# Kernel tuning notes

Measured on AMD Instinct MI355X. Metric: run time of the kernel, lower is better.

The kernel has to match this reference:

```python
import jax, jax.numpy as jnp
import numpy as np

B, T, C, H = 4, 2048, 1024, 16
D = C // H  # head_dim = 64


def setup_inputs() -> dict:
    key = jax.random.key(0)
    k1, k2, k3 = jax.random.split(key, 3)
    x = jax.random.normal(k1, (B, T, C), dtype=jnp.float32)
    w_attn = jax.random.normal(k2, (C, 3 * C), dtype=jnp.float32) * (1.0 / np.sqrt(C))
    b_attn = jnp.zeros((3 * C,), dtype=jnp.float32)
    w_proj = jax.random.normal(k3, (C, C), dtype=jnp.float32) * (1.0 / np.sqrt(C))
    b_proj = jnp.zeros((C,), dtype=jnp.float32)
    return {"x": x, "w_attn": w_attn, "b_attn": b_attn, "w_proj": w_proj, "b_proj": b_proj}


def reference(x, w_attn, b_attn, w_proj, b_proj):
    Bx, Tx, Cx = x.shape
    qkv = x @ w_attn + b_attn                      # (B, T, 3C)
    q, k, v = jnp.split(qkv, 3, axis=2)
    # (B, T, C) -> (B, H, T, D)
    q = q.reshape(Bx, Tx, H, D).transpose(0, 2, 1, 3)
    k = k.reshape(Bx, Tx, H, D).transpose(0, 2, 1, 3)
    v = v.reshape(Bx, Tx, H, D).transpose(0, 2, 1, 3)
    scores = jnp.einsum('bhqd,bhkd->bhqk', q, k) / jnp.sqrt(jnp.float32(D))
    causal = jnp.tril(jnp.ones((Tx, Tx), dtype=bool))
    scores = jnp.where(causal[None, None], scores, jnp.float32(-jnp.inf))
    probs = jax.nn.softmax(scores, axis=-1)
    out = jnp.einsum('bhqk,bhkd->bhqd', probs, v)  # (B, H, T, D)
    out = out.transpose(0, 2, 1, 3).reshape(Bx, Tx, Cx)
    return out @ w_proj + b_proj
```

## Files before the change

kernel.cpp:

```cpp
#include <hip/hip_runtime.h>

#define AS1 __attribute__((address_space(1)))
#define AS3 __attribute__((address_space(3)))

using bf16x8  = __attribute__((ext_vector_type(8))) __bf16;
using floatx4 = __attribute__((ext_vector_type(4))) float;

#define SCQ 0.18033688f

__device__ inline ushort f2b(float f) {
    __bf16 h = (__bf16)f;
    return __builtin_bit_cast(ushort, h);
}

__global__ void k_conv(const float* __restrict__ in, ushort* __restrict__ out, int n) {
    int i = (blockIdx.x * 256 + threadIdx.x) * 4;
    if (i < n) {
        float4 v = *(const float4*)(in + i);
        ushort4 o;
        o.x = f2b(v.x); o.y = f2b(v.y); o.z = f2b(v.z); o.w = f2b(v.w);
        *(ushort4*)(out + i) = o;
    }
}

__global__ void k_transpose(const float* __restrict__ in, ushort* __restrict__ out,
                            int R, int Ncol, float scale, int scale_cols) {
    __shared__ float tile[32][33];
    int tx = threadIdx.x & 31, ty = threadIdx.x >> 5;
    int c0 = blockIdx.x * 32, r0 = blockIdx.y * 32;
    for (int i = 0; i < 32; i += 8)
        tile[ty + i][tx] = in[(size_t)(r0 + ty + i) * Ncol + c0 + tx];
    __syncthreads();
    for (int i = 0; i < 32; i += 8) {
        int n = c0 + ty + i;
        float v = tile[tx][ty + i];
        if (n < scale_cols) v *= scale;
        out[(size_t)n * R + r0 + tx] = f2b(v);
    }
}

__global__ __launch_bounds__(256, 2) void k_gemm_bt(
    const ushort* __restrict__ A, const ushort* __restrict__ Bt,
    const float* __restrict__ bias, float* __restrict__ outv,
    int M, int N, int K)
{
    __shared__ __align__(16) ushort As[128 * 32];
    __shared__ __align__(16) ushort Bs[128 * 32];
    int tid = threadIdx.x;
    int m0 = blockIdx.y * 128, n0 = blockIdx.x * 128;
    int lane = tid & 63;
    int wm = (tid >> 7) * 64;
    int wn = ((tid >> 6) & 1) * 64;
    int lr = lane & 15, quad = lane >> 4, lk = quad * 8;

    floatx4 acc[4][4] = {};
    const ushort* ag = A  + (size_t)(m0 + (tid >> 2)) * K + (tid & 3) * 8;
    const ushort* bg = Bt + (size_t)(n0 + (tid >> 2)) * K + (tid & 3) * 8;
    ushort* asd = &As[tid * 8];
    ushort* bsd = &Bs[tid * 8];

    for (int kt = 0; kt < K; kt += 32) {
        __builtin_amdgcn_global_load_lds((const AS1 unsigned int*)(ag + kt),                  (AS3 unsigned int*)(asd),        16, 0, 0);
        __builtin_amdgcn_global_load_lds((const AS1 unsigned int*)(ag + kt + (size_t)64 * K), (AS3 unsigned int*)(asd + 2048), 16, 0, 0);
        __builtin_amdgcn_global_load_lds((const AS1 unsigned int*)(bg + kt),                  (AS3 unsigned int*)(bsd),        16, 0, 0);
        __builtin_amdgcn_global_load_lds((const AS1 unsigned int*)(bg + kt + (size_t)64 * K), (AS3 unsigned int*)(bsd + 2048), 16, 0, 0);
        asm volatile("s_waitcnt vmcnt(0)" ::: "memory");
        __syncthreads();
        bf16x8 af[4], bf[4];
        #pragma unroll
        for (int i = 0; i < 4; ++i) af[i] = *(const bf16x8*)&As[(wm + 16 * i + lr) * 32 + lk];
        #pragma unroll
        for (int j = 0; j < 4; ++j) bf[j] = *(const bf16x8*)&Bs[(wn + 16 * j + lr) * 32 + lk];
        #pragma unroll
        for (int i = 0; i < 4; ++i)
            #pragma unroll
            for (int j = 0; j < 4; ++j)
                acc[i][j] = __builtin_amdgcn_mfma_f32_16x16x32_bf16(af[i], bf[j], acc[i][j], 0, 0, 0);
        __syncthreads();
    }

    #pragma unroll
    for (int j = 0; j < 4; ++j) {
        int col = n0 + wn + 16 * j + lr;
        float bv = bias[col];
        #pragma unroll
        for (int i = 0; i < 4; ++i) {
            int row = m0 + wm + 16 * i + quad * 4;
            #pragma unroll
            for (int r = 0; r < 4; ++r)
                outv[(size_t)(row + r) * N + col] = acc[i][j][r] + bv;
        }
    }
}

__global__ __launch_bounds__(256, 2) void k_gemm_qkv(
    const ushort* __restrict__ A, const ushort* __restrict__ Bt,
    const float* __restrict__ bias, ushort* __restrict__ qkv, ushort* __restrict__ vt)
{
    constexpr int K = 1024;
    __shared__ __align__(16) ushort As[128 * 32];
    __shared__ __align__(16) ushort Bs[128 * 32];
    int tid = threadIdx.x;
    int m0 = blockIdx.y * 128, n0 = blockIdx.x * 128;
    int lane = tid & 63;
    int wm = (tid >> 7) * 64;
    int wn = ((tid >> 6) & 1) * 64;
    int lr = lane & 15, quad = lane >> 4, lk = quad * 8;

    floatx4 acc[4][4] = {};
    const ushort* ag = A  + (size_t)(m0 + (tid >> 2)) * K + (tid & 3) * 8;
    const ushort* bg = Bt + (size_t)(n0 + (tid >> 2)) * K + (tid & 3) * 8;
    ushort* asd = &As[tid * 8];
    ushort* bsd = &Bs[tid * 8];

    for (int kt = 0; kt < K; kt += 32) {
        __builtin_amdgcn_global_load_lds((const AS1 unsigned int*)(ag + kt),                  (AS3 unsigned int*)(asd),        16, 0, 0);
        __builtin_amdgcn_global_load_lds((const AS1 unsigned int*)(ag + kt + (size_t)64 * K), (AS3 unsigned int*)(asd + 2048), 16, 0, 0);
        __builtin_amdgcn_global_load_lds((const AS1 unsigned int*)(bg + kt),                  (AS3 unsigned int*)(bsd),        16, 0, 0);
        __builtin_amdgcn_global_load_lds((const AS1 unsigned int*)(bg + kt + (size_t)64 * K), (AS3 unsigned int*)(bsd + 2048), 16, 0, 0);
        asm volatile("s_waitcnt vmcnt(0)" ::: "memory");
        __syncthreads();
        bf16x8 af[4], bf[4];
        #pragma unroll
        for (int i = 0; i < 4; ++i) af[i] = *(const bf16x8*)&As[(wm + 16 * i + lr) * 32 + lk];
        #pragma unroll
        for (int j = 0; j < 4; ++j) bf[j] = *(const bf16x8*)&Bs[(wn + 16 * j + lr) * 32 + lk];
        #pragma unroll
        for (int i = 0; i < 4; ++i)
            #pragma unroll
            for (int j = 0; j < 4; ++j)
                acc[i][j] = __builtin_amdgcn_mfma_f32_16x16x32_bf16(af[i], bf[j], acc[i][j], 0, 0, 0);
        __syncthreads();
    }

    int bb = m0 >> 11;
    #pragma unroll
    for (int j = 0; j < 4; ++j) {
        int col = n0 + wn + 16 * j + lr;
        float bv = bias[col];
        if (col < 1024) bv *= SCQ;
        if (col < 2048) {
            #pragma unroll
            for (int i = 0; i < 4; ++i) {
                int row = m0 + wm + 16 * i + quad * 4;
                #pragma unroll
                for (int r = 0; r < 4; ++r)
                    qkv[(size_t)(row + r) * 2048 + col] = f2b(acc[i][j][r] + bv);
            }
        } else {
            int h = (col - 2048) >> 6, d = (col - 2048) & 63;
            ushort* vbase = vt + ((size_t)(bb * 16 + h) * 64 + d) * 2048;
            #pragma unroll
            for (int i = 0; i < 4; ++i) {
                int t0 = (m0 + wm + 16 * i + quad * 4) & 2047;
                ushort4 pk;
                ((ushort*)&pk)[0] = f2b(acc[i][j][0] + bv);
                ((ushort*)&pk)[1] = f2b(acc[i][j][1] + bv);
                ((ushort*)&pk)[2] = f2b(acc[i][j][2] + bv);
                ((ushort*)&pk)[3] = f2b(acc[i][j][3] + bv);
                *(ushort4*)&vbase[t0] = pk;
            }
        }
    }
}

__global__ __launch_bounds__(512, 4) void k_attn(const ushort* __restrict__ qkv,
                                                 const ushort* __restrict__ vt,
                                                 ushort* __restrict__ out)
{
    constexpr int T = 2048, SQK = 2048, C = 1024;
    __shared__ __align__(16) ushort Ks[2 * 64 * 64];
    __shared__ __align__(16) ushort Vs[2 * 64 * 64];
    __shared__ __align__(16) ushort Ps[8 * 16 * 72];
    int tid = threadIdx.x;
    int lane = tid & 63, wave = tid >> 6;
    int lr = lane & 15, quad = lane >> 4, lk = quad * 8;
    int bh = blockIdx.y;
    int b = bh >> 4, h = bh & 15;
    size_t base = (size_t)b * T * SQK;
    const ushort* kg0 = qkv + base + 1024 + h * 64;
    const ushort* vg0 = vt + (size_t)bh * 64 * 2048;
    ushort* psw = &Ps[wave * 16 * 72];

    int srow = tid >> 3;
    int sg   = (tid & 7) ^ (srow & 7);
    const ushort* kgs = kg0 + (size_t)srow * SQK + sg * 8;
    const ushort* vgs = vg0 + (size_t)srow * 2048 + sg * 8;

    bf16x8 ones;
    #pragma unroll
    for (int i = 0; i < 8; ++i) ones[i] = (__bf16)1.0f;
    int c0 = (quad ^ (lr & 7)) * 8;
    int c1 = ((4 + quad) ^ (lr & 7)) * 8;

    int qts[2] = { (int)blockIdx.x, 15 - (int)blockIdx.x };
    for (int ti = 0; ti < 2; ++ti) {
        int qt = qts[ti];
        int qrow = qt * 128 + wave * 16;
        int kt_d = qrow >> 6;
        int qoff = (qrow & 63) + lr;
        const ushort* qp = qkv + base + (size_t)(qrow + lr) * SQK + h * 64;
        bf16x8 aq0 = *(const bf16x8*)(qp + lk);
        bf16x8 aq1 = *(const bf16x8*)(qp + 32 + lk);
        floatx4 o[4] = {};
        floatx4 lacc = {};
        int ktmax = 2 * qt + 1;

        __syncthreads();
        __builtin_amdgcn_global_load_lds((const AS1 unsigned int*)(kgs),
                                         (AS3 unsigned int*)&Ks[tid * 8], 16, 0, 0);
        __builtin_amdgcn_global_load_lds((const AS1 unsigned int*)(vgs),
                                         (AS3 unsigned int*)&Vs[tid * 8], 16, 0, 0);

        for (int kt = 0; kt <= ktmax; ++kt) {
            int cur = kt & 1;
            asm volatile("s_waitcnt vmcnt(0)" ::: "memory");
            __syncthreads();
            if (kt < ktmax) {
                int nb = cur ^ 1;
                __builtin_amdgcn_global_load_lds(
                    (const AS1 unsigned int*)(kgs + (size_t)(kt + 1) * 64 * SQK),
                    (AS3 unsigned int*)&Ks[nb * 4096 + tid * 8], 16, 0, 0);
                __builtin_amdgcn_global_load_lds(
                    (const AS1 unsigned int*)(vgs + (kt + 1) * 64),
                    (AS3 unsigned int*)&Vs[nb * 4096 + tid * 8], 16, 0, 0);
            }
            if (kt > kt_d) continue;
            const ushort* Kb = &Ks[cur * 4096];
            const ushort* Vb = &Vs[cur * 4096];
            bool diag = (kt == kt_d);

            #pragma unroll
            for (int jk = 0; jk < 4; ++jk) {
                const ushort* kr = &Kb[(16 * jk + lr) * 64];
                bf16x8 ak0 = *(const bf16x8*)(kr + c0);
                bf16x8 ak1 = *(const bf16x8*)(kr + c1);
                floatx4 z = {};
                floatx4 st = __builtin_amdgcn_mfma_f32_16x16x32_bf16(ak0, aq0, z, 0, 0, 0);
                st = __builtin_amdgcn_mfma_f32_16x16x32_bf16(ak1, aq1, st, 0, 0, 0);
                int kloc = 16 * jk + quad * 4;
                uint2 w;
                if (diag) {
                    float p0 = (kloc + 0 > qoff) ? 0.f : exp2f(st[0]);
                    float p1 = (kloc + 1 > qoff) ? 0.f : exp2f(st[1]);
                    float p2 = (kloc + 2 > qoff) ? 0.f : exp2f(st[2]);
                    float p3 = (kloc + 3 > qoff) ? 0.f : exp2f(st[3]);
                    w.x = (unsigned)f2b(p0) | ((unsigned)f2b(p1) << 16);
                    w.y = (unsigned)f2b(p2) | ((unsigned)f2b(p3) << 16);
                } else {
                    w.x = (unsigned)f2b(exp2f(st[0])) | ((unsigned)f2b(exp2f(st[1])) << 16);
                    w.y = (unsigned)f2b(exp2f(st[2])) | ((unsigned)f2b(exp2f(st[3])) << 16);
                }
                *(uint2*)&psw[lr * 72 + kloc] = w;
            }
            asm volatile("s_waitcnt lgkmcnt(0)" ::: "memory");
            bf16x8 ap0 = *(const bf16x8*)&psw[lr * 72 + lk];
            bf16x8 ap1 = *(const bf16x8*)&psw[lr * 72 + 32 + lk];
            lacc = __builtin_amdgcn_mfma_f32_16x16x32_bf16(ap0, ones, lacc, 0, 0, 0);
            lacc = __builtin_amdgcn_mfma_f32_16x16x32_bf16(ap1, ones, lacc, 0, 0, 0);
            #pragma unroll
            for (int jd = 0; jd < 4; ++jd) {
                const ushort* vr = &Vb[(16 * jd + lr) * 64];
                bf16x8 bv0 = *(const bf16x8*)(vr + c0);
                bf16x8 bv1 = *(const bf16x8*)(vr + c1);
                o[jd] = __builtin_amdgcn_mfma_f32_16x16x32_bf16(ap0, bv0, o[jd], 0, 0, 0);
                o[jd] = __builtin_amdgcn_mfma_f32_16x16x32_bf16(ap1, bv1, o[jd], 0, 0, 0);
            }
        }

        #pragma unroll
        for (int r = 0; r < 4; ++r) {
            float inv = 1.0f / lacc[r];
            int row = b * T + qrow + quad * 4 + r;
            #pragma unroll
            for (int jd = 0; jd < 4; ++jd)
                out[(size_t)row * C + h * 64 + 16 * jd + lr] = f2b(o[jd][r] * inv);
        }
    }
}

extern "C" void kernel_launch(void* const* d_in, const int* in_sizes, int n_in,
                              void* d_out, int out_size, void* d_ws, size_t ws_size,
                              hipStream_t stream) {
    const float* x      = (const float*)d_in[0];
    const float* w_attn = (const float*)d_in[1];
    const float* b_attn = (const float*)d_in[2];
    const float* w_proj = (const float*)d_in[3];
    const float* b_proj = (const float*)d_in[4];
    float* out = (float*)d_out;

    constexpr int Bb = 4, T = 2048, C = 1024;
    constexpr int M = Bb * T;

    ushort* xb  = (ushort*)d_ws;
    ushort* waT = xb  + (size_t)M * C;
    ushort* wpT = waT + (size_t)3 * C * C;
    ushort* qkv = wpT + (size_t)C * C;
    ushort* vt  = qkv + (size_t)M * 2 * C;
    ushort* ao  = vt  + (size_t)64 * 64 * T;

    k_conv<<<(M * C / 4 + 255) / 256, 256, 0, stream>>>(x, xb, M * C);
    k_transpose<<<dim3(3 * C / 32, C / 32), 256, 0, stream>>>(w_attn, waT, C, 3 * C, SCQ, C);
    k_transpose<<<dim3(C / 32, C / 32), 256, 0, stream>>>(w_proj, wpT, C, C, 1.0f, 0);
    k_gemm_qkv<<<dim3(3 * C / 128, M / 128), 256, 0, stream>>>(xb, waT, b_attn, qkv, vt);
    k_attn<<<dim3(8, Bb * 16), 512, 0, stream>>>(qkv, vt, ao);
    k_gemm_bt<<<dim3(C / 128, M / 128), 256, 0, stream>>>(ao, wpT, b_proj, out, M, C, C);
}
```

Before: 267.7 us.

## Shrink attention q-tile to 64 rows and keep P in registers via 16x16x16 MFMA

```diff
diff --git a/kernel.cpp b/kernel.cpp
--- a/kernel.cpp
+++ b/kernel.cpp
@@ -5,8 +5,15 @@
 
 using bf16x8  = __attribute__((ext_vector_type(8))) __bf16;
 using floatx4 = __attribute__((ext_vector_type(4))) float;
+using short4v = __attribute__((ext_vector_type(4))) short;
 
 #define SCQ 0.18033688f
+
+#if __has_builtin(__builtin_amdgcn_mfma_f32_16x16x16bf16_1k)
+#define HAVE_MFMA16 1
+#else
+#define HAVE_MFMA16 0
+#endif
 
 __device__ inline ushort f2b(float f) {
     __bf16 h = (__bf16)f;
@@ -164,14 +171,16 @@
     }
 }
 
-__global__ __launch_bounds__(512, 4) void k_attn(const ushort* __restrict__ qkv,
+__global__ __launch_bounds__(256, 4) void k_attn(const ushort* __restrict__ qkv,
                                                  const ushort* __restrict__ vt,
                                                  ushort* __restrict__ out)
 {
     constexpr int T = 2048, SQK = 2048, C = 1024;
     __shared__ __align__(16) ushort Ks[2 * 64 * 64];
     __shared__ __align__(16) ushort Vs[2 * 64 * 64];
-    __shared__ __align__(16) ushort Ps[8 * 16 * 72];
+#if !HAVE_MFMA16
+    __shared__ __align__(16) ushort Ps[4 * 16 * 72];
+#endif
     int tid = threadIdx.x;
     int lane = tid & 63, wave = tid >> 6;
     int lr = lane & 15, quad = lane >> 4, lk = quad * 8;
@@ -180,55 +189,60 @@
     size_t base = (size_t)b * T * SQK;
     const ushort* kg0 = qkv + base + 1024 + h * 64;
     const ushort* vg0 = vt + (size_t)bh * 64 * 2048;
-    ushort* psw = &Ps[wave * 16 * 72];
-
-    int srow = tid >> 3;
-    int sg   = (tid & 7) ^ (srow & 7);
-    const ushort* kgs = kg0 + (size_t)srow * SQK + sg * 8;
-    const ushort* vgs = vg0 + (size_t)srow * 2048 + sg * 8;
-
-    bf16x8 ones;
+
+    const ushort* kgs[2]; const ushort* vgs[2]; int sdst[2];
     #pragma unroll
-    for (int i = 0; i < 8; ++i) ones[i] = (__bf16)1.0f;
+    for (int it = 0; it < 2; ++it) {
+        int s = tid + 256 * it;
+        int row = s >> 3, g = (s & 7) ^ (row & 7);
+        kgs[it] = kg0 + (size_t)row * SQK + g * 8;
+        vgs[it] = vg0 + (size_t)row * 2048 + g * 8;
+        sdst[it] = s * 8;
+    }
+
     int c0 = (quad ^ (lr & 7)) * 8;
     int c1 = ((4 + quad) ^ (lr & 7)) * 8;
-
-    int qts[2] = { (int)blockIdx.x, 15 - (int)blockIdx.x };
+    short4v ones4 = { 0x3F80, 0x3F80, 0x3F80, 0x3F80 };
+
+    int qts[2] = { (int)blockIdx.x, 31 - (int)blockIdx.x };
     for (int ti = 0; ti < 2; ++ti) {
         int qt = qts[ti];
-        int qrow = qt * 128 + wave * 16;
-        int kt_d = qrow >> 6;
-        int qoff = (qrow & 63) + lr;
+        int qrow = qt * 64 + wave * 16;
         const ushort* qp = qkv + base + (size_t)(qrow + lr) * SQK + h * 64;
         bf16x8 aq0 = *(const bf16x8*)(qp + lk);
         bf16x8 aq1 = *(const bf16x8*)(qp + 32 + lk);
         floatx4 o[4] = {};
         floatx4 lacc = {};
-        int ktmax = 2 * qt + 1;
-
-        __syncthreads();
-        __builtin_amdgcn_global_load_lds((const AS1 unsigned int*)(kgs),
-                                         (AS3 unsigned int*)&Ks[tid * 8], 16, 0, 0);
-        __builtin_amdgcn_global_load_lds((const AS1 unsigned int*)(vgs),
-                                         (AS3 unsigned int*)&Vs[tid * 8], 16, 0, 0);
-
-        for (int kt = 0; kt <= ktmax; ++kt) {
+
+        __syncthreads();
+        #pragma unroll
+        for (int it = 0; it < 2; ++it) {
+            __builtin_amdgcn_global_load_lds((const AS1 unsigned int*)(kgs[it]),
+                                             (AS3 unsigned int*)&Ks[sdst[it]], 16, 0, 0);
+            __builtin_amdgcn_global_load_lds((const AS1 unsigned int*)(vgs[it]),
+                                             (AS3 unsigned int*)&Vs[sdst[it]], 16, 0, 0);
+        }
+
+        for (int kt = 0; kt <= qt; ++kt) {
             int cur = kt & 1;
             asm volatile("s_waitcnt vmcnt(0)" ::: "memory");
             __syncthreads();
-            if (kt < ktmax) {
-                int nb = cur ^ 1;
-                __builtin_amdgcn_global_load_lds(
-                    (const AS1 unsigned int*)(kgs + (size_t)(kt + 1) * 64 * SQK),
-                    (AS3 unsigned int*)&Ks[nb * 4096 + tid * 8], 16, 0, 0);
-                __builtin_amdgcn_global_load_lds(
-                    (const AS1 unsigned int*)(vgs + (kt + 1) * 64),
-                    (AS3 unsigned int*)&Vs[nb * 4096 + tid * 8], 16, 0, 0);
-            }
-            if (kt > kt_d) continue;
+            if (kt < qt) {
+                int nb = (cur ^ 1) * 4096;
+                #pragma unroll
+                for (int it = 0; it < 2; ++it) {
+                    __builtin_amdgcn_global_load_lds(
+                        (const AS1 unsigned int*)(kgs[it] + (size_t)(kt + 1) * 64 * SQK),
+                        (AS3 unsigned int*)&Ks[nb + sdst[it]], 16, 0, 0);
+                    __builtin_amdgcn_global_load_lds(
+                        (const AS1 unsigned int*)(vgs[it] + (kt + 1) * 64),
+                        (AS3 unsigned int*)&Vs[nb + sdst[it]], 16, 0, 0);
+                }
+            }
             const ushort* Kb = &Ks[cur * 4096];
             const ushort* Vb = &Vs[cur * 4096];
-            bool diag = (kt == kt_d);
+            bool diag = (kt == qt);
+            int qloc = wave * 16 + lr;
 
             #pragma unroll
             for (int jk = 0; jk < 4; ++jk) {
@@ -239,33 +253,54 @@
                 floatx4 st = __builtin_amdgcn_mfma_f32_16x16x32_bf16(ak0, aq0, z, 0, 0, 0);
                 st = __builtin_amdgcn_mfma_f32_16x16x32_bf16(ak1, aq1, st, 0, 0, 0);
                 int kloc = 16 * jk + quad * 4;
+                float e0, e1, e2, e3;
+                if (diag) {
+                    e0 = (kloc + 0 > qloc) ? 0.f : exp2f(st[0]);
+                    e1 = (kloc + 1 > qloc) ? 0.f : exp2f(st[1]);
+                    e2 = (kloc + 2 > qloc) ? 0.f : exp2f(st[2]);
+                    e3 = (kloc + 3 > qloc) ? 0.f : exp2f(st[3]);
+                } else {
+                    e0 = exp2f(st[0]); e1 = exp2f(st[1]);
+                    e2 = exp2f(st[2]); e3 = exp2f(st[3]);
+                }
+#if HAVE_MFMA16
+                short4v ap;
+                ap[0] = (short)f2b(e0); ap[1] = (short)f2b(e1);
+                ap[2] = (short)f2b(e2); ap[3] = (short)f2b(e3);
+                lacc = __builtin_amdgcn_mfma_f32_16x16x16bf16_1k(ap, ones4, lacc, 0, 0, 0);
+                #pragma unroll
+                for (int jd = 0; jd < 4; ++jd) {
+                    int p = (2 * jk + (quad >> 1)) ^ (lr & 7);
+                    short4v bv = *(const short4v*)&Vb[(16 * jd + lr) * 64 + p * 8 + (quad & 1) * 4];
+                    o[jd] = __builtin_amdgcn_mfma_f32_16x16x16bf16_1k(ap, bv, o[jd], 0, 0, 0);
+                }
+#else
                 uint2 w;
-                if (diag) {
-                    float p0 = (kloc + 0 > qoff) ? 0.f : exp2f(st[0]);
-                    float p1 = (kloc + 1 > qoff) ? 0.f : exp2f(st[1]);
-                    float p2 = (kloc + 2 > qoff) ? 0.f : exp2f(st[2]);
-                    float p3 = (kloc + 3 > qoff) ? 0.f : exp2f(st[3]);
-                    w.x = (unsigned)f2b(p0) | ((unsigned)f2b(p1) << 16);
-                    w.y = (unsigned)f2b(p2) | ((unsigned)f2b(p3) << 16);
-                } else {
-                    w.x = (unsigned)f2b(exp2f(st[0])) | ((unsigned)f2b(exp2f(st[1])) << 16);
-                    w.y = (unsigned)f2b(exp2f(st[2])) | ((unsigned)f2b(exp2f(st[3])) << 16);
+                w.x = (unsigned)f2b(e0) | ((unsigned)f2b(e1) << 16);
+                w.y = (unsigned)f2b(e2) | ((unsigned)f2b(e3) << 16);
+                *(uint2*)&Ps[(wave * 16 + lr) * 72 + kloc] = w;
+#endif
+            }
+#if !HAVE_MFMA16
+            asm volatile("s_waitcnt lgkmcnt(0)" ::: "memory");
+            {
+                bf16x8 ones;
+                #pragma unroll
+                for (int i = 0; i < 8; ++i) ones[i] = (__bf16)1.0f;
+                bf16x8 ap0 = *(const bf16x8*)&Ps[(wave * 16 + lr) * 72 + lk];
+                bf16x8 ap1 = *(const bf16x8*)&Ps[(wave * 16 + lr) * 72 + 32 + lk];
+                lacc = __builtin_amdgcn_mfma_f32_16x16x32_bf16(ap0, ones, lacc, 0, 0, 0);
+                lacc = __builtin_amdgcn_mfma_f32_16x16x32_bf16(ap1, ones, lacc, 0, 0, 0);
+                #pragma unroll
+                for (int jd = 0; jd < 4; ++jd) {
+                    const ushort* vr = &Vb[(16 * jd + lr) * 64];
+                    bf16x8 bv0 = *(const bf16x8*)(vr + c0);
+                    bf16x8 bv1 = *(const bf16x8*)(vr + c1);
+                    o[jd] = __builtin_amdgcn_mfma_f32_16x16x32_bf16(ap0, bv0, o[jd], 0, 0, 0);
+                    o[jd] = __builtin_amdgcn_mfma_f32_16x16x32_bf16(ap1, bv1, o[jd], 0, 0, 0);
                 }
-                *(uint2*)&psw[lr * 72 + kloc] = w;
-            }
-            asm volatile("s_waitcnt lgkmcnt(0)" ::: "memory");
-            bf16x8 ap0 = *(const bf16x8*)&psw[lr * 72 + lk];
-            bf16x8 ap1 = *(const bf16x8*)&psw[lr * 72 + 32 + lk];
-            lacc = __builtin_amdgcn_mfma_f32_16x16x32_bf16(ap0, ones, lacc, 0, 0, 0);
-            lacc = __builtin_amdgcn_mfma_f32_16x16x32_bf16(ap1, ones, lacc, 0, 0, 0);
-            #pragma unroll
-            for (int jd = 0; jd < 4; ++jd) {
-                const ushort* vr = &Vb[(16 * jd + lr) * 64];
-                bf16x8 bv0 = *(const bf16x8*)(vr + c0);
-                bf16x8 bv1 = *(const bf16x8*)(vr + c1);
-                o[jd] = __builtin_amdgcn_mfma_f32_16x16x32_bf16(ap0, bv0, o[jd], 0, 0, 0);
-                o[jd] = __builtin_amdgcn_mfma_f32_16x16x32_bf16(ap1, bv1, o[jd], 0, 0, 0);
-            }
+            }
+#endif
         }
 
         #pragma unroll
@@ -303,6 +338,6 @@
     k_transpose<<<dim3(3 * C / 32, C / 32), 256, 0, stream>>>(w_attn, waT, C, 3 * C, SCQ, C);
     k_transpose<<<dim3(C / 32, C / 32), 256, 0, stream>>>(w_proj, wpT, C, C, 1.0f, 0);
     k_gemm_qkv<<<dim3(3 * C / 128, M / 128), 256, 0, stream>>>(xb, waT, b_attn, qkv, vt);
-    k_attn<<<dim3(8, Bb * 16), 512, 0, stream>>>(qkv, vt, ao);
+    k_attn<<<dim3(16, Bb * 16), 256, 0, stream>>>(qkv, vt, ao);
     k_gemm_bt<<<dim3(C / 128, M / 128), 256, 0, stream>>>(ao, wpT, b_proj, out, M, C, C);
 }
```

Result: slower. 287.0 us (+7.2%).
